# Kernel tuning notes

Hardware: AMD Instinct MI355X
Metric: run time of the kernel (lower is better)

The kernel has to match this reference:

```python
import jax, jax.numpy as jnp
import numpy as np

B = 1_000_000          # query points
D = 3                  # n_input_dims
N_LEVELS = 16
MIN_RES, MAX_RES = 16, 512
N_ENC = 2 ** 19        # max hashmap entries per level
N_EMBED = 2
INIT_SCALE = 1e-4
PRIMES = (1, 2654435761, 805459861)  # instant-ngp spatial-hash primes


def _resolutions():
    # Eq. 2/3 of instant-ngp: geometric growth from MIN_RES to MAX_RES
    growth = np.exp((np.log(MAX_RES) - np.log(MIN_RES)) / (N_LEVELS - 1))
    return [int(np.floor(MIN_RES * growth ** l)) for l in range(N_LEVELS)]

RES = _resolutions()
LEVEL_N_ENC = [min(r ** D, N_ENC) for r in RES]
LEVEL_HASH = [r ** D > N_ENC for r in RES]          # hash iff grid overflows table
CORNERS = np.stack(np.meshgrid(*([np.arange(2)] * D), indexing='ij'), -1).reshape(-1, D)  # (8,3)


def setup_inputs() -> dict:
    key = jax.random.key(0)
    ks = jax.random.split(key, N_LEVELS + 1)
    inp = {"x": jax.random.uniform(ks[0], (B, D), minval=-1.0, maxval=1.0, dtype=jnp.float32)}
    for l in range(N_LEVELS):
        inp[f"emb{l}"] = jax.random.uniform(
            ks[l + 1], (LEVEL_N_ENC[l], N_EMBED), minval=-INIT_SCALE, maxval=INIT_SCALE, dtype=jnp.float32
        )
    return inp


def _level_features(x, emb, res, n_enc, use_hash):
    # x: (B,3) in [-1,1] -> pixel coords, align_corners=False convention
    xp = (x + 1.0) * (res * 0.5) - 0.5
    x0 = jnp.floor(xp)
    t = xp - x0                                           # (B,3) fractional part
    ci = jnp.asarray(CORNERS, jnp.int32)                  # (8,3) corner offsets
    c = x0.astype(jnp.int32)[:, None, :] + ci[None]       # (B,8,3) corner coords
    off = jnp.asarray(CORNERS, xp.dtype)
    # trilinear weights: prod over dims of t or (1-t)
    w = jnp.prod(jnp.where(off[None] > 0, t[:, None, :], 1.0 - t[:, None, :]), axis=-1)  # (B,8)
    m = jnp.all((c >= 0) & (c < res), axis=-1)            # (B,8) zeros-padding mask
    if use_hash:
        cu = c.astype(jnp.uint32)
        h = cu[..., 0] * jnp.uint32(PRIMES[0])
        for d in range(1, D):
            h = h ^ (cu[..., d] * jnp.uint32(PRIMES[d]))
        ids = (h % jnp.uint32(n_enc)).astype(jnp.int32)
    else:
        # ravel index, x varies fastest ('xy' grid indexing)
        ids = (c[..., 0] + c[..., 1] * res + c[..., 2] * res * res) % n_enc
    ids = jnp.where(m, ids, 0)
    w = jnp.where(m, w, jnp.zeros_like(w))
    return jnp.sum(emb[ids] * w[..., None], axis=1)       # (B,E)


def reference(x, emb0, emb1, emb2, emb3, emb4, emb5, emb6, emb7,
              emb8, emb9, emb10, emb11, emb12, emb13, emb14, emb15):
    embs = [emb0, emb1, emb2, emb3, emb4, emb5, emb6, emb7,
            emb8, emb9, emb10, emb11, emb12, emb13, emb14, emb15]
    feats = [_level_features(x, embs[l], RES[l], LEVEL_N_ENC[l], LEVEL_HASH[l])
             for l in range(N_LEVELS)]
    return jnp.stack(feats, axis=1)  # (B, L, E)
```

## Files before the change

### kernel.cpp

```cpp
#include <hip/hip_runtime.h>
#include <stdint.h>


struct EmbPtrs { const float2* p[16]; };

constexpr int BLOCK  = 256;
constexpr int DBLOCK = 1024;
constexpr int L0N = 16*16*16;
constexpr int L1N = 20*20*20;
constexpr int kRes[16] = {16,20,25,32,40,50,64,80,101,128,161,203,256,322,406,512};
constexpr uint32_t P1 = 2654435761u, P2 = 805459861u;
constexpr uint32_t HMASK = (1u << 19) - 1u;

struct Tri {
    int ix, iy, iz;
    float wx[2], wy[2], wz[2];
    bool vx[2], vy[2], vz[2];
};

template<int RES_>
__device__ __forceinline__ Tri tri_setup(float px, float py, float pz)
{
    Tri s;
    const float rh = (float)RES_ * 0.5f;
    const float xp = (px + 1.0f) * rh - 0.5f;
    const float yp = (py + 1.0f) * rh - 0.5f;
    const float zp = (pz + 1.0f) * rh - 0.5f;
    const float fx = floorf(xp), fy = floorf(yp), fz = floorf(zp);
    s.ix = (int)fx; s.iy = (int)fy; s.iz = (int)fz;
    const float tx = xp - fx, ty = yp - fy, tz = zp - fz;
    s.wx[0] = 1.0f - tx; s.wx[1] = tx;
    s.wy[0] = 1.0f - ty; s.wy[1] = ty;
    s.wz[0] = 1.0f - tz; s.wz[1] = tz;
    s.vx[0] = (s.ix   >= 0) && (s.ix   < RES_); s.vx[1] = (s.ix+1 >= 0) && (s.ix+1 < RES_);
    s.vy[0] = (s.iy   >= 0) && (s.iy   < RES_); s.vy[1] = (s.iy+1 >= 0) && (s.iy+1 < RES_);
    s.vz[0] = (s.iz   >= 0) && (s.iz   < RES_); s.vz[1] = (s.iz+1 >= 0) && (s.iz+1 < RES_);
    return s;
}

template<int RES_, typename PTR>
__device__ __forceinline__ float2 dense_feat(PTR tab, float px, float py, float pz)
{
    const Tri s = tri_setup<RES_>(px, py, pz);
    constexpr int r2 = RES_ * RES_;
    const int base = s.ix + s.iy * RES_ + s.iz * r2;
    float ax = 0.0f, ay = 0.0f;
#pragma unroll
    for (int k = 0; k < 2; ++k)
#pragma unroll
    for (int j = 0; j < 2; ++j)
#pragma unroll
    for (int i = 0; i < 2; ++i) {
        const bool v = s.vx[i] && s.vy[j] && s.vz[k];
        const uint32_t idx = v ? (uint32_t)(base + i + j*RES_ + k*r2) : 0u;
        const float w = v ? (s.wx[i]*s.wy[j]*s.wz[k]) : 0.0f;
        const float2 e = tab[idx];
        ax = fmaf(e.x, w, ax);
        ay = fmaf(e.y, w, ay);
    }
    return make_float2(ax, ay);
}

template<int RES_>
__device__ __forceinline__ float2 hash_feat(const float2* __restrict__ tab,
                                            float px, float py, float pz)
{
    const Tri s = tri_setup<RES_>(px, py, pz);
    const uint32_t hy0 = (uint32_t)s.iy * P1;
    const uint32_t hz0 = (uint32_t)s.iz * P2;
    const uint32_t hx[2] = {(uint32_t)s.ix, (uint32_t)s.ix + 1u};
    const uint32_t hy[2] = {hy0, hy0 + P1};
    const uint32_t hz[2] = {hz0, hz0 + P2};
    float ax = 0.0f, ay = 0.0f;
#pragma unroll
    for (int k = 0; k < 2; ++k)
#pragma unroll
    for (int j = 0; j < 2; ++j)
#pragma unroll
    for (int i = 0; i < 2; ++i) {
        const bool v = s.vx[i] && s.vy[j] && s.vz[k];
        uint32_t idx = (hx[i] ^ hy[j] ^ hz[k]) & HMASK;
        idx = v ? idx : 0u;
        const float w = v ? (s.wx[i]*s.wy[j]*s.wz[k]) : 0.0f;
        const float2 e = tab[idx];
        ax = fmaf(e.x, w, ax);
        ay = fmaf(e.y, w, ay);
    }
    return make_float2(ax, ay);
}

__global__ __launch_bounds__(DBLOCK) void dense_kernel(
    const float* __restrict__ x, EmbPtrs embs, float4* __restrict__ out, int n)
{
    __shared__ float2 lds0[L0N];
    __shared__ float2 lds1[L1N];

    {
        const float4* g0 = (const float4*)embs.p[0];
        const float4* g1 = (const float4*)embs.p[1];
        float4* s0 = (float4*)lds0;
        float4* s1 = (float4*)lds1;
#pragma unroll 2
        for (int i = threadIdx.x; i < L0N/2; i += DBLOCK) s0[i] = g0[i];
#pragma unroll 4
        for (int i = threadIdx.x; i < L1N/2; i += DBLOCK) s1[i] = g1[i];
    }
    __syncthreads();

    const int b = blockIdx.x * DBLOCK + threadIdx.x;
    if (b >= n) return;
    const float px = x[3*b+0], py = x[3*b+1], pz = x[3*b+2];

    float2 f[8];
    f[0] = dense_feat<16>((const float2*)lds0, px, py, pz);
    f[1] = dense_feat<20>((const float2*)lds1, px, py, pz);
    f[2] = dense_feat<25>(embs.p[2], px, py, pz);
    f[3] = dense_feat<32>(embs.p[3], px, py, pz);
    f[4] = dense_feat<40>(embs.p[4], px, py, pz);
    f[5] = dense_feat<50>(embs.p[5], px, py, pz);
    f[6] = dense_feat<64>(embs.p[6], px, py, pz);
    f[7] = dense_feat<80>(embs.p[7], px, py, pz);

    float4* o = out + (size_t)b * 8;
#pragma unroll
    for (int i = 0; i < 4; ++i)
        o[i] = make_float4(f[2*i].x, f[2*i].y, f[2*i+1].x, f[2*i+1].y);
}

template<int L>
__global__ __launch_bounds__(BLOCK) void hash_level_kernel(
    const float* __restrict__ x, const float2* __restrict__ tab,
    float2* __restrict__ ws, int n)
{
    const int b = blockIdx.x * BLOCK + threadIdx.x;
    if (b >= n) return;
    ws[b] = hash_feat<kRes[L]>(tab, x[3*b+0], x[3*b+1], x[3*b+2]);
}

__global__ __launch_bounds__(BLOCK) void merge_kernel(
    const float2* __restrict__ ws, float4* __restrict__ out, int n)
{
    const int b = blockIdx.x * BLOCK + threadIdx.x;
    if (b >= n) return;
    float2 f[8];
#pragma unroll
    for (int l = 0; l < 8; ++l)
        f[l] = ws[(size_t)l * n + b];
    float4* o = out + (size_t)b * 8 + 4;
#pragma unroll
    for (int i = 0; i < 4; ++i)
        o[i] = make_float4(f[2*i].x, f[2*i].y, f[2*i+1].x, f[2*i+1].y);
}

__global__ __launch_bounds__(BLOCK) void fallback_kernel(
    const float* __restrict__ x, EmbPtrs embs, float4* __restrict__ out, int n)
{
    const int b = blockIdx.x * BLOCK + threadIdx.x;
    if (b >= n) return;
    const float px = x[3*b+0], py = x[3*b+1], pz = x[3*b+2];
    float2 f[16];
    f[0]  = dense_feat<16 >(embs.p[0],  px, py, pz);
    f[1]  = dense_feat<20 >(embs.p[1],  px, py, pz);
    f[2]  = dense_feat<25 >(embs.p[2],  px, py, pz);
    f[3]  = dense_feat<32 >(embs.p[3],  px, py, pz);
    f[4]  = dense_feat<40 >(embs.p[4],  px, py, pz);
    f[5]  = dense_feat<50 >(embs.p[5],  px, py, pz);
    f[6]  = dense_feat<64 >(embs.p[6],  px, py, pz);
    f[7]  = dense_feat<80 >(embs.p[7],  px, py, pz);
    f[8]  = hash_feat<101>(embs.p[8],  px, py, pz);
    f[9]  = hash_feat<128>(embs.p[9],  px, py, pz);
    f[10] = hash_feat<161>(embs.p[10], px, py, pz);
    f[11] = hash_feat<203>(embs.p[11], px, py, pz);
    f[12] = hash_feat<256>(embs.p[12], px, py, pz);
    f[13] = hash_feat<322>(embs.p[13], px, py, pz);
    f[14] = hash_feat<406>(embs.p[14], px, py, pz);
    f[15] = hash_feat<512>(embs.p[15], px, py, pz);
    float4* o = out + (size_t)b * 8;
#pragma unroll
    for (int i = 0; i < 8; ++i)
        o[i] = make_float4(f[2*i].x, f[2*i].y, f[2*i+1].x, f[2*i+1].y);
}

extern "C" void kernel_launch(void* const* d_in, const int* in_sizes, int n_in,
                              void* d_out, int out_size, void* d_ws, size_t ws_size,
                              hipStream_t stream) {
    const float* x = (const float*)d_in[0];
    EmbPtrs embs;
    for (int l = 0; l < 16; ++l) embs.p[l] = (const float2*)d_in[1 + l];
    const int n = in_sizes[0] / 3;
    const int grid  = (n + BLOCK - 1) / BLOCK;
    const int dgrid = (n + DBLOCK - 1) / DBLOCK;
    float4* out = (float4*)d_out;

    const size_t need = (size_t)8 * (size_t)n * sizeof(float2);
    if (ws_size >= need) {
        float2* ws = (float2*)d_ws;
        dense_kernel<<<dgrid, DBLOCK, 0, stream>>>(x, embs, out, n);
        hash_level_kernel< 8><<<grid, BLOCK, 0, stream>>>(x, embs.p[ 8], ws + 0*(size_t)n, n);
        hash_level_kernel< 9><<<grid, BLOCK, 0, stream>>>(x, embs.p[ 9], ws + 1*(size_t)n, n);
        hash_level_kernel<10><<<grid, BLOCK, 0, stream>>>(x, embs.p[10], ws + 2*(size_t)n, n);
        hash_level_kernel<11><<<grid, BLOCK, 0, stream>>>(x, embs.p[11], ws + 3*(size_t)n, n);
        hash_level_kernel<12><<<grid, BLOCK, 0, stream>>>(x, embs.p[12], ws + 4*(size_t)n, n);
        hash_level_kernel<13><<<grid, BLOCK, 0, stream>>>(x, embs.p[13], ws + 5*(size_t)n, n);
        hash_level_kernel<14><<<grid, BLOCK, 0, stream>>>(x, embs.p[14], ws + 6*(size_t)n, n);
        hash_level_kernel<15><<<grid, BLOCK, 0, stream>>>(x, embs.p[15], ws + 7*(size_t)n, n);
        merge_kernel<<<grid, BLOCK, 0, stream>>>(ws, out, n);
    } else {
        fallback_kernel<<<grid, BLOCK, 0, stream>>>(x, embs, out, n);
    }
}
```

Baseline: 636.0 us.

## Repack dense level tables into x-pair float4 rows and double hash work per thread

Adds repack kernels that copy dense levels 2-7 into a float4 table in which each entry also holds its x+1 neighbour. Trilinear lookups then need four 16-byte gathers per level instead of eight 8-byte ones. Each hash-level thread now handles two points, half the batch apart, so more independent gathers are in flight per thread. The cost is six extra launches that repack each call and about 12 MB of added workspace. A fallback path is kept for when the workspace is too small.

After: 656.0 us. +3.2%, slower.

```diff
diff --git a/kernel.cpp b/kernel.cpp
--- a/kernel.cpp
+++ b/kernel.cpp
@@ -3,12 +3,14 @@
 
 
 struct EmbPtrs { const float2* p[16]; };
+struct PkPtrs  { const float4* p[6];  };
 
 constexpr int BLOCK  = 256;
 constexpr int DBLOCK = 1024;
 constexpr int L0N = 16*16*16;
 constexpr int L1N = 20*20*20;
 constexpr int kRes[16] = {16,20,25,32,40,50,64,80,101,128,161,203,256,322,406,512};
+constexpr int kPkEnt[6] = {25*25*25, 32*32*32, 40*40*40, 50*50*50, 64*64*64, 80*80*80};
 constexpr uint32_t P1 = 2654435761u, P2 = 805459861u;
 constexpr uint32_t HMASK = (1u << 19) - 1u;
 
@@ -62,6 +64,34 @@
 }
 
 template<int RES_>
+__device__ __forceinline__ float2 dense_feat_pk(const float4* __restrict__ tab,
+                                                float px, float py, float pz)
+{
+    const Tri s = tri_setup<RES_>(px, py, pz);
+    constexpr int r2 = RES_ * RES_;
+    constexpr int NE = RES_ * r2;
+    const int shift = (s.ix < 0) ? 1 : 0;
+    float ax = 0.0f, ay = 0.0f;
+#pragma unroll
+    for (int k = 0; k < 2; ++k)
+#pragma unroll
+    for (int j = 0; j < 2; ++j) {
+        const bool vyz = s.vy[j] && s.vz[k];
+        const float wyz = s.wy[j] * s.wz[k];
+        const float w0 = (vyz && s.vx[0]) ? s.wx[0] * wyz : 0.0f;
+        const float w1 = (vyz && s.vx[1]) ? s.wx[1] * wyz : 0.0f;
+        int a = s.ix + shift + (s.iy + j) * RES_ + (s.iz + k) * r2;
+        a = min(max(a, 0), NE - 1);
+        const float4 q = tab[a];
+        const float wA = shift ? w1 : w0;
+        const float wB = shift ? 0.0f : w1;
+        ax = fmaf(q.x, wA, ax); ay = fmaf(q.y, wA, ay);
+        ax = fmaf(q.z, wB, ax); ay = fmaf(q.w, wB, ay);
+    }
+    return make_float2(ax, ay);
+}
+
+template<int RES_>
 __device__ __forceinline__ float2 hash_feat(const float2* __restrict__ tab,
                                             float px, float py, float pz)
 {
@@ -89,12 +119,23 @@
     return make_float2(ax, ay);
 }
 
-__global__ __launch_bounds__(DBLOCK) void dense_kernel(
-    const float* __restrict__ x, EmbPtrs embs, float4* __restrict__ out, int n)
+template<int NE>
+__global__ __launch_bounds__(BLOCK) void repack_kernel(
+    const float2* __restrict__ t, float4* __restrict__ r)
+{
+    const int i = blockIdx.x * BLOCK + threadIdx.x;
+    if (i >= NE) return;
+    const float2 a = t[i];
+    const float2 b = t[(i + 1 < NE) ? i + 1 : i];
+    r[i] = make_float4(a.x, a.y, b.x, b.y);
+}
+
+__global__ __launch_bounds__(DBLOCK) void dense_kernel_pk(
+    const float* __restrict__ x, EmbPtrs embs, PkPtrs pk,
+    float4* __restrict__ out, int n)
 {
     __shared__ float2 lds0[L0N];
     __shared__ float2 lds1[L1N];
-
     {
         const float4* g0 = (const float4*)embs.p[0];
         const float4* g1 = (const float4*)embs.p[1];
@@ -114,6 +155,43 @@
     float2 f[8];
     f[0] = dense_feat<16>((const float2*)lds0, px, py, pz);
     f[1] = dense_feat<20>((const float2*)lds1, px, py, pz);
+    f[2] = dense_feat_pk<25>(pk.p[0], px, py, pz);
+    f[3] = dense_feat_pk<32>(pk.p[1], px, py, pz);
+    f[4] = dense_feat_pk<40>(pk.p[2], px, py, pz);
+    f[5] = dense_feat_pk<50>(pk.p[3], px, py, pz);
+    f[6] = dense_feat_pk<64>(pk.p[4], px, py, pz);
+    f[7] = dense_feat_pk<80>(pk.p[5], px, py, pz);
+
+    float4* o = out + (size_t)b * 8;
+#pragma unroll
+    for (int i = 0; i < 4; ++i)
+        o[i] = make_float4(f[2*i].x, f[2*i].y, f[2*i+1].x, f[2*i+1].y);
+}
+
+__global__ __launch_bounds__(DBLOCK) void dense_kernel(
+    const float* __restrict__ x, EmbPtrs embs, float4* __restrict__ out, int n)
+{
+    __shared__ float2 lds0[L0N];
+    __shared__ float2 lds1[L1N];
+    {
+        const float4* g0 = (const float4*)embs.p[0];
+        const float4* g1 = (const float4*)embs.p[1];
+        float4* s0 = (float4*)lds0;
+        float4* s1 = (float4*)lds1;
+#pragma unroll 2
+        for (int i = threadIdx.x; i < L0N/2; i += DBLOCK) s0[i] = g0[i];
+#pragma unroll 4
+        for (int i = threadIdx.x; i < L1N/2; i += DBLOCK) s1[i] = g1[i];
+    }
+    __syncthreads();
+
+    const int b = blockIdx.x * DBLOCK + threadIdx.x;
+    if (b >= n) return;
+    const float px = x[3*b+0], py = x[3*b+1], pz = x[3*b+2];
+
+    float2 f[8];
+    f[0] = dense_feat<16>((const float2*)lds0, px, py, pz);
+    f[1] = dense_feat<20>((const float2*)lds1, px, py, pz);
     f[2] = dense_feat<25>(embs.p[2], px, py, pz);
     f[3] = dense_feat<32>(embs.p[3], px, py, pz);
     f[4] = dense_feat<40>(embs.p[4], px, py, pz);
@@ -132,9 +210,15 @@
     const float* __restrict__ x, const float2* __restrict__ tab,
     float2* __restrict__ ws, int n)
 {
+    const int h = (n + 1) >> 1;
     const int b = blockIdx.x * BLOCK + threadIdx.x;
-    if (b >= n) return;
-    ws[b] = hash_feat<kRes[L]>(tab, x[3*b+0], x[3*b+1], x[3*b+2]);
+    if (b >= h) return;
+    const int p1 = b + h;
+    const int q1 = (p1 < n) ? p1 : b;
+    const float2 r0 = hash_feat<kRes[L]>(tab, x[3*b+0],  x[3*b+1],  x[3*b+2]);
+    const float2 r1 = hash_feat<kRes[L]>(tab, x[3*q1+0], x[3*q1+1], x[3*q1+2]);
+    ws[b] = r0;
+    if (p1 < n) ws[p1] = r1;
 }
 
 __global__ __launch_bounds__(BLOCK) void merge_kernel(
@@ -189,21 +273,50 @@
     for (int l = 0; l < 16; ++l) embs.p[l] = (const float2*)d_in[1 + l];
     const int n = in_sizes[0] / 3;
     const int grid  = (n + BLOCK - 1) / BLOCK;
+    const int hgrid = (((n + 1) >> 1) + BLOCK - 1) / BLOCK;
     const int dgrid = (n + DBLOCK - 1) / DBLOCK;
     float4* out = (float4*)d_out;
 
-    const size_t need = (size_t)8 * (size_t)n * sizeof(float2);
-    if (ws_size >= need) {
+    const size_t hashBytes = (size_t)8 * (size_t)n * sizeof(float2);
+    size_t pkBytes = 0;
+    for (int i = 0; i < 6; ++i) pkBytes += (size_t)kPkEnt[i] * sizeof(float4);
+
+    if (ws_size >= hashBytes + pkBytes) {
+        float2* ws = (float2*)d_ws;
+        char* base = (char*)d_ws + hashBytes;
+        float4* pkp[6];
+        size_t off = 0;
+        for (int i = 0; i < 6; ++i) { pkp[i] = (float4*)(base + off); off += (size_t)kPkEnt[i] * sizeof(float4); }
+        PkPtrs pk; for (int i = 0; i < 6; ++i) pk.p[i] = pkp[i];
+
+        repack_kernel<kPkEnt[0]><<<(kPkEnt[0]+BLOCK-1)/BLOCK, BLOCK, 0, stream>>>(embs.p[2], pkp[0]);
+        repack_kernel<kPkEnt[1]><<<(kPkEnt[1]+BLOCK-1)/BLOCK, BLOCK, 0, stream>>>(embs.p[3], pkp[1]);
+        repack_kernel<kPkEnt[2]><<<(kPkEnt[2]+BLOCK-1)/BLOCK, BLOCK, 0, stream>>>(embs.p[4], pkp[2]);
+        repack_kernel<kPkEnt[3]><<<(kPkEnt[3]+BLOCK-1)/BLOCK, BLOCK, 0, stream>>>(embs.p[5], pkp[3]);
+        repack_kernel<kPkEnt[4]><<<(kPkEnt[4]+BLOCK-1)/BLOCK, BLOCK, 0, stream>>>(embs.p[6], pkp[4]);
+        repack_kernel<kPkEnt[5]><<<(kPkEnt[5]+BLOCK-1)/BLOCK, BLOCK, 0, stream>>>(embs.p[7], pkp[5]);
+
+        dense_kernel_pk<<<dgrid, DBLOCK, 0, stream>>>(x, embs, pk, out, n);
+        hash_level_kernel< 8><<<hgrid, BLOCK, 0, stream>>>(x, embs.p[ 8], ws + 0*(size_t)n, n);
+        hash_level_kernel< 9><<<hgrid, BLOCK, 0, stream>>>(x, embs.p[ 9], ws + 1*(size_t)n, n);
+        hash_level_kernel<10><<<hgrid, BLOCK, 0, stream>>>(x, embs.p[10], ws + 2*(size_t)n, n);
+        hash_level_kernel<11><<<hgrid, BLOCK, 0, stream>>>(x, embs.p[11], ws + 3*(size_t)n, n);
+        hash_level_kernel<12><<<hgrid, BLOCK, 0, stream>>>(x, embs.p[12], ws + 4*(size_t)n, n);
+        hash_level_kernel<13><<<hgrid, BLOCK, 0, stream>>>(x, embs.p[13], ws + 5*(size_t)n, n);
+        hash_level_kernel<14><<<hgrid, BLOCK, 0, stream>>>(x, embs.p[14], ws + 6*(size_t)n, n);
+        hash_level_kernel<15><<<hgrid, BLOCK, 0, stream>>>(x, embs.p[15], ws + 7*(size_t)n, n);
+        merge_kernel<<<grid, BLOCK, 0, stream>>>(ws, out, n);
+    } else if (ws_size >= hashBytes) {
         float2* ws = (float2*)d_ws;
         dense_kernel<<<dgrid, DBLOCK, 0, stream>>>(x, embs, out, n);
-        hash_level_kernel< 8><<<grid, BLOCK, 0, stream>>>(x, embs.p[ 8], ws + 0*(size_t)n, n);
-        hash_level_kernel< 9><<<grid, BLOCK, 0, stream>>>(x, embs.p[ 9], ws + 1*(size_t)n, n);
-        hash_level_kernel<10><<<grid, BLOCK, 0, stream>>>(x, embs.p[10], ws + 2*(size_t)n, n);
-        hash_level_kernel<11><<<grid, BLOCK, 0, stream>>>(x, embs.p[11], ws + 3*(size_t)n, n);
-        hash_level_kernel<12><<<grid, BLOCK, 0, stream>>>(x, embs.p[12], ws + 4*(size_t)n, n);
-        hash_level_kernel<13><<<grid, BLOCK, 0, stream>>>(x, embs.p[13], ws + 5*(size_t)n, n);
-        hash_level_kernel<14><<<grid, BLOCK, 0, stream>>>(x, embs.p[14], ws + 6*(size_t)n, n);
-        hash_level_kernel<15><<<grid, BLOCK, 0, stream>>>(x, embs.p[15], ws + 7*(size_t)n, n);
+        hash_level_kernel< 8><<<hgrid, BLOCK, 0, stream>>>(x, embs.p[ 8], ws + 0*(size_t)n, n);
+        hash_level_kernel< 9><<<hgrid, BLOCK, 0, stream>>>(x, embs.p[ 9], ws + 1*(size_t)n, n);
+        hash_level_kernel<10><<<hgrid, BLOCK, 0, stream>>>(x, embs.p[10], ws + 2*(size_t)n, n);
+        hash_level_kernel<11><<<hgrid, BLOCK, 0, stream>>>(x, embs.p[11], ws + 3*(size_t)n, n);
+        hash_level_kernel<12><<<hgrid, BLOCK, 0, stream>>>(x, embs.p[12], ws + 4*(size_t)n, n);
+        hash_level_kernel<13><<<hgrid, BLOCK, 0, stream>>>(x, embs.p[13], ws + 5*(size_t)n, n);
+        hash_level_kernel<14><<<hgrid, BLOCK, 0, stream>>>(x, embs.p[14], ws + 6*(size_t)n, n);
+        hash_level_kernel<15><<<hgrid, BLOCK, 0, stream>>>(x, embs.p[15], ws + 7*(size_t)n, n);
         merge_kernel<<<grid, BLOCK, 0, stream>>>(ws, out, n);
     } else {
         fallback_kernel<<<grid, BLOCK, 0, stream>>>(x, embs, out, n);
```

## Sort query points into Morton-ordered spatial bins before dense-level gathers

Applied to the files above, without the earlier changes.

Adds a counting sort of the query points into 32^3 Morton-ordered bins (histogram, single-block scan, atomic scatter) and runs the dense-level kernel on the sorted points. Nearby threads then touch nearby table entries, which improves cache locality of the gathers. Outputs are written back through the stored original index, so the output writes become scattered. The hash levels still read the unsorted points. The cost is four extra passes over the input plus atomics, and only the dense levels benefit.

After: 645.0 us. No clear change (+1.4%).

```diff
diff --git a/kernel.cpp b/kernel.cpp
--- a/kernel.cpp
+++ b/kernel.cpp
@@ -8,6 +8,7 @@
 constexpr int DBLOCK = 1024;
 constexpr int L0N = 16*16*16;
 constexpr int L1N = 20*20*20;
+constexpr int NBINS = 32768;
 constexpr int kRes[16] = {16,20,25,32,40,50,64,80,101,128,161,203,256,322,406,512};
 constexpr uint32_t P1 = 2654435761u, P2 = 805459861u;
 constexpr uint32_t HMASK = (1u << 19) - 1u;
@@ -89,12 +90,108 @@
     return make_float2(ax, ay);
 }
 
+__device__ __forceinline__ uint32_t part1by2(uint32_t v)
+{
+    v = (v | (v << 16)) & 0x030000FFu;
+    v = (v | (v << 8))  & 0x0300F00Fu;
+    v = (v | (v << 4))  & 0x030C30C3u;
+    v = (v | (v << 2))  & 0x09249249u;
+    return v;
+}
+
+__device__ __forceinline__ uint32_t bin_of(float x, float y, float z)
+{
+    const int bx = min(max((int)((x + 1.0f) * 16.0f), 0), 31);
+    const int by = min(max((int)((y + 1.0f) * 16.0f), 0), 31);
+    const int bz = min(max((int)((z + 1.0f) * 16.0f), 0), 31);
+    return part1by2((uint32_t)bx) | (part1by2((uint32_t)by) << 1) | (part1by2((uint32_t)bz) << 2);
+}
+
+__global__ __launch_bounds__(BLOCK) void hist_kernel(
+    const float* __restrict__ x, uint32_t* __restrict__ hist, int n)
+{
+    const int b = blockIdx.x * BLOCK + threadIdx.x;
+    if (b >= n) return;
+    atomicAdd(&hist[bin_of(x[3*b+0], x[3*b+1], x[3*b+2])], 1u);
+}
+
+__global__ __launch_bounds__(1024) void scan_kernel(
+    const uint32_t* __restrict__ hist, uint32_t* __restrict__ cursor)
+{
+    __shared__ uint32_t tot[1024];
+    const int t = threadIdx.x;
+    uint32_t v[32];
+    uint32_t s = 0;
+#pragma unroll
+    for (int i = 0; i < 32; ++i) { v[i] = s; s += hist[t*32 + i]; }
+    tot[t] = s;
+    __syncthreads();
+    for (int off = 1; off < 1024; off <<= 1) {
+        const uint32_t y = (t >= off) ? tot[t - off] : 0u;
+        __syncthreads();
+        tot[t] += y;
+        __syncthreads();
+    }
+    const uint32_t base = tot[t] - s;
+#pragma unroll
+    for (int i = 0; i < 32; ++i) cursor[t*32 + i] = base + v[i];
+}
+
+__global__ __launch_bounds__(BLOCK) void scatter_kernel(
+    const float* __restrict__ x, uint32_t* __restrict__ cursor,
+    float4* __restrict__ xs, int n)
+{
+    const int b = blockIdx.x * BLOCK + threadIdx.x;
+    if (b >= n) return;
+    const float px = x[3*b+0], py = x[3*b+1], pz = x[3*b+2];
+    const uint32_t pos = atomicAdd(&cursor[bin_of(px, py, pz)], 1u);
+    xs[pos] = make_float4(px, py, pz, __int_as_float(b));
+}
+
+__global__ __launch_bounds__(DBLOCK) void dense_kernel_binned(
+    const float4* __restrict__ xs, EmbPtrs embs, float4* __restrict__ out, int n)
+{
+    __shared__ float2 lds0[L0N];
+    __shared__ float2 lds1[L1N];
+    {
+        const float4* g0 = (const float4*)embs.p[0];
+        const float4* g1 = (const float4*)embs.p[1];
+        float4* s0 = (float4*)lds0;
+        float4* s1 = (float4*)lds1;
+#pragma unroll 2
+        for (int i = threadIdx.x; i < L0N/2; i += DBLOCK) s0[i] = g0[i];
+#pragma unroll 4
+        for (int i = threadIdx.x; i < L1N/2; i += DBLOCK) s1[i] = g1[i];
+    }
+    __syncthreads();
+
+    const int i = blockIdx.x * DBLOCK + threadIdx.x;
+    if (i >= n) return;
+    const float4 q = xs[i];
+    const float px = q.x, py = q.y, pz = q.z;
+    const int idx = __float_as_int(q.w);
+
+    float2 f[8];
+    f[0] = dense_feat<16>((const float2*)lds0, px, py, pz);
+    f[1] = dense_feat<20>((const float2*)lds1, px, py, pz);
+    f[2] = dense_feat<25>(embs.p[2], px, py, pz);
+    f[3] = dense_feat<32>(embs.p[3], px, py, pz);
+    f[4] = dense_feat<40>(embs.p[4], px, py, pz);
+    f[5] = dense_feat<50>(embs.p[5], px, py, pz);
+    f[6] = dense_feat<64>(embs.p[6], px, py, pz);
+    f[7] = dense_feat<80>(embs.p[7], px, py, pz);
+
+    float4* o = out + (size_t)idx * 8;
+#pragma unroll
+    for (int k = 0; k < 4; ++k)
+        o[k] = make_float4(f[2*k].x, f[2*k].y, f[2*k+1].x, f[2*k+1].y);
+}
+
 __global__ __launch_bounds__(DBLOCK) void dense_kernel(
     const float* __restrict__ x, EmbPtrs embs, float4* __restrict__ out, int n)
 {
     __shared__ float2 lds0[L0N];
     __shared__ float2 lds1[L1N];
-
     {
         const float4* g0 = (const float4*)embs.p[0];
         const float4* g1 = (const float4*)embs.p[1];
@@ -192,8 +289,34 @@
     const int dgrid = (n + DBLOCK - 1) / DBLOCK;
     float4* out = (float4*)d_out;
 
-    const size_t need = (size_t)8 * (size_t)n * sizeof(float2);
-    if (ws_size >= need) {
+    const size_t streamsB = (size_t)8 * (size_t)n * sizeof(float2);
+    const size_t xsB      = (size_t)n * sizeof(float4);
+    const size_t histB    = (size_t)NBINS * sizeof(uint32_t);
+    const size_t needBin  = streamsB + xsB + 2 * histB;
+    const size_t needR9   = streamsB;
+
+    if (ws_size >= needBin) {
+        float2*   ws     = (float2*)d_ws;
+        float4*   xs     = (float4*)((char*)d_ws + streamsB);
+        uint32_t* hist   = (uint32_t*)((char*)d_ws + streamsB + xsB);
+        uint32_t* cursor = hist + NBINS;
+
+        hipMemsetAsync(hist, 0, histB, stream);
+        hist_kernel<<<grid, BLOCK, 0, stream>>>(x, hist, n);
+        scan_kernel<<<1, 1024, 0, stream>>>(hist, cursor);
+        scatter_kernel<<<grid, BLOCK, 0, stream>>>(x, cursor, xs, n);
+
+        dense_kernel_binned<<<dgrid, DBLOCK, 0, stream>>>(xs, embs, out, n);
+        hash_level_kernel< 8><<<grid, BLOCK, 0, stream>>>(x, embs.p[ 8], ws + 0*(size_t)n, n);
+        hash_level_kernel< 9><<<grid, BLOCK, 0, stream>>>(x, embs.p[ 9], ws + 1*(size_t)n, n);
+        hash_level_kernel<10><<<grid, BLOCK, 0, stream>>>(x, embs.p[10], ws + 2*(size_t)n, n);
+        hash_level_kernel<11><<<grid, BLOCK, 0, stream>>>(x, embs.p[11], ws + 3*(size_t)n, n);
+        hash_level_kernel<12><<<grid, BLOCK, 0, stream>>>(x, embs.p[12], ws + 4*(size_t)n, n);
+        hash_level_kernel<13><<<grid, BLOCK, 0, stream>>>(x, embs.p[13], ws + 5*(size_t)n, n);
+        hash_level_kernel<14><<<grid, BLOCK, 0, stream>>>(x, embs.p[14], ws + 6*(size_t)n, n);
+        hash_level_kernel<15><<<grid, BLOCK, 0, stream>>>(x, embs.p[15], ws + 7*(size_t)n, n);
+        merge_kernel<<<grid, BLOCK, 0, stream>>>(ws, out, n);
+    } else if (ws_size >= needR9) {
         float2* ws = (float2*)d_ws;
         dense_kernel<<<dgrid, DBLOCK, 0, stream>>>(x, embs, out, n);
         hash_level_kernel< 8><<<grid, BLOCK, 0, stream>>>(x, embs.p[ 8], ws + 0*(size_t)n, n);
```
